# Kernel tuning notes

Measured on AMD Instinct MI355X. Metric: run time of the kernel, lower is better.

## Reference

```python
import jax, jax.numpy as jnp
import numpy as np

NUM_ITERS = 2  # quasi-DEER fixed-point iterations (module default num_iters=2)


def _affine_scan(A, b):
    """Parallel first-order linear recurrence h_t = A_t*h_{t-1} + b_t along axis=1.
    A, b: (B, T, H). Equivalent to torch accelerated-scan after removing pow-2 padding."""
    def comb(l, r):
        A1, b1 = l
        A2, b2 = r
        return A2 * A1, A2 * b1 + b2
    return jax.lax.associative_scan(comb, (A, b), axis=1)[1]


def _run_direction(x, W_in, b_in, W_rec, U_z, b_u, num_iters):
    """quasi-DEER evaluation of a MinRNN layer.
    x: (B, T, d_in). Returns states (B, T, H). Initial state h0 = 0 (hx=None)."""
    B, T, _ = x.shape
    H = b_in.shape[0]
    dtype = x.dtype
    h0 = jnp.zeros((B, H), dtype)
    diag_rec = jnp.diagonal(W_rec)  # (H,)
    # z depends only on the input, not on the state -> precompute once.
    z = jnp.tanh(jnp.einsum('bti,hi->bth', x, W_in) + b_in)  # (B, T, H)
    z0, z_rest = z[:, 0], z[:, 1:]
    states = jnp.zeros((B, T, H), dtype)
    for _ in range(num_iters):
        h_prev = states[:, :-1]  # (B, T-1, H), paired with inputs[:,1:]
        u = jax.nn.sigmoid(jnp.einsum('bth,gh->btg', h_prev, W_rec)
                           + jnp.einsum('bth,gh->btg', z_rest, U_z) + b_u)
        fs = u * h_prev + (1.0 - u) * z_rest                      # cell output f
        As = u + (h_prev - z_rest) * u * (1.0 - u) * diag_rec     # diagonal Jacobian
        bs = fs - As * h_prev
        u0 = jax.nn.sigmoid(h0 @ W_rec.T + z0 @ U_z.T + b_u)
        b0 = u0 * h0 + (1.0 - u0) * z0                            # f(x_0, h0)
        A = jnp.concatenate([jnp.zeros_like(b0)[:, None], As], axis=1)  # A0 = 0
        b = jnp.concatenate([b0[:, None], bs], axis=1)
        states = _affine_scan(A, b)
    return states


def _prnn_forward(input, Wf_in, bf_in, Wf_rec, Uf_z, bf_u,
                  Wb_in, bb_in, Wb_rec, Ub_z, bb_u):
    fwd = _run_direction(input, Wf_in, bf_in, Wf_rec, Uf_z, bf_u, NUM_ITERS)
    bwd = _run_direction(input[:, ::-1], Wb_in, bb_in, Wb_rec, Ub_z, bb_u, NUM_ITERS)[:, ::-1]
    output = jnp.concatenate([fwd, bwd], axis=2)      # (B, T, 2H)
    h_n = jnp.stack([fwd[:, -1], bwd[:, 0]])          # (2, B, H)
    return output, h_n


def setup_inputs() -> dict:
    key = jax.random.key(0)
    ks = jax.random.split(key, 12)
    B, T, D_IN, H = 8, 8192, 256, 256
    def minrnn_params(k0, k1, k2, d_in, h):
        kw, kr, ku = k0, k1, k2
        return dict(
            W_in=jax.random.normal(kw, (h, d_in), jnp.float32) / d_in ** 0.5,
            b_in=jnp.zeros((h,), jnp.float32),
            W_rec=jax.random.normal(kr, (h, h), jnp.float32) / h ** 0.5,
            U_z=jax.random.normal(ku, (h, h), jnp.float32) / h ** 0.5,
            b_u=jnp.zeros((h,), jnp.float32),
        )
    pf = minrnn_params(ks[0], ks[1], ks[2], D_IN, H)
    pb = minrnn_params(ks[3], ks[4], ks[5], D_IN, H)
    return {
        'input': jax.random.normal(ks[6], (B, T, D_IN), jnp.float32),
        'Wf_in': pf['W_in'], 'bf_in': pf['b_in'], 'Wf_rec': pf['W_rec'],
        'Uf_z': pf['U_z'], 'bf_u': pf['b_u'],
        'Wb_in': pb['W_in'], 'bb_in': pb['b_in'], 'Wb_rec': pb['W_rec'],
        'Ub_z': pb['U_z'], 'bb_u': pb['b_u'],
    }


def reference(input, Wf_in, bf_in, Wf_rec, Uf_z, bf_u,
              Wb_in, bb_in, Wb_rec, Ub_z, bb_u):
    return _prnn_forward(input, Wf_in, bf_in, Wf_rec, Uf_z, bf_u,
                         Wb_in, bb_in, Wb_rec, Ub_z, bb_u)
```

## Files before the change

### kernel.cpp

```cpp
#include <hip/hip_runtime.h>
#include <stdint.h>

typedef unsigned short u16;
typedef __attribute__((ext_vector_type(8))) short short8v;
typedef __attribute__((ext_vector_type(4))) short short4v;
typedef __attribute__((ext_vector_type(4))) float f32x4;

#define B_ 8
#define T_ 8192
#define H_ 256
#define M_ 65536
#define MH 16777216
#define NCH 256
#define CHL 32
#define NCHAN 4096

__device__ __forceinline__ u16 f2bf(float f) {
  union { float f; uint32_t u; } v; v.f = f;
  return (u16)((v.u + 0x7FFFu + ((v.u >> 16) & 1u)) >> 16);
}
__device__ __forceinline__ float bf2f(u16 s) {
  union { uint32_t u; float f; } v; v.u = ((uint32_t)s) << 16;
  return v.f;
}
__device__ __forceinline__ float sigm(float x) {
  return __fdividef(1.0f, 1.0f + __expf(-x));
}
__device__ __forceinline__ float tanhfast(float x) {
  return 1.0f - __fdividef(2.0f, __expf(2.0f * x) + 1.0f);
}

__device__ __forceinline__ void compute_Ab(float zf, float ag, float hp, float dr,
                                           float& Aa, float& bb) {
  const float u = sigm(ag);
  const float g = u * (1.f - u) * dr;
  Aa = u + (hp - zf) * g;
  bb = u * hp + (1.f - u) * zf - Aa * hp;
}

__device__ __forceinline__ void g2l16(const void* g, void* l) {
  __builtin_amdgcn_global_load_lds((const __attribute__((address_space(1))) void*)g,
                                   (__attribute__((address_space(3))) void*)l, 16, 0, 0);
}
__device__ __forceinline__ int zts(int row, int col) {
  return row * 256 + ((((col >> 3) ^ (row & 7)) << 3) | (col & 7));
}

__global__ __launch_bounds__(256) void prep_kernel(
    const float* __restrict__ x, u16* __restrict__ xf,
    const float* __restrict__ w0, const float* __restrict__ w1, const float* __restrict__ w2,
    const float* __restrict__ w3, const float* __restrict__ w4, const float* __restrict__ w5,
    u16* __restrict__ wbf) {
  const int bx = blockIdx.x;
  const float* src;
  u16* dst;
  size_t i;
  if (bx < 8192) {
    i = ((size_t)bx * 256 + threadIdx.x) * 8;
    src = x; dst = xf;
  } else {
    const int r = bx - 8192;
    const int wsel = r >> 5, blk = r & 31;
    src = (wsel == 0) ? w0 : (wsel == 1) ? w1 : (wsel == 2) ? w2
        : (wsel == 3) ? w3 : (wsel == 4) ? w4 : w5;
    dst = wbf + (size_t)wsel * 65536;
    i = ((size_t)blk * 256 + threadIdx.x) * 8;
  }
  const float4* s4 = (const float4*)(src + i);
  float4 a = s4[0], b = s4[1];
  short8v o;
  o[0] = (short)f2bf(a.x); o[1] = (short)f2bf(a.y);
  o[2] = (short)f2bf(a.z); o[3] = (short)f2bf(a.w);
  o[4] = (short)f2bf(b.x); o[5] = (short)f2bf(b.y);
  o[6] = (short)f2bf(b.z); o[7] = (short)f2bf(b.w);
  *(short8v*)(dst + i) = o;
}

__global__ __launch_bounds__(256) void zzu_k(
    const u16* __restrict__ xf, const u16* __restrict__ wbf,
    const float* __restrict__ bin0, const float* __restrict__ bin1,
    const float* __restrict__ bu0, const float* __restrict__ bu1,
    const float* __restrict__ Wf_rec, const float* __restrict__ Wb_rec,
    u16* __restrict__ zout, u16* __restrict__ zuout,
    float* __restrict__ Pout, float* __restrict__ qout) {
  __shared__ __align__(16) char lds[65536];
  const int dir = blockIdx.z;
  const int tm = blockIdx.x;
  const char* Win = (const char*)(wbf + (size_t)dir * 196608);
  const char* Uz  = (const char*)(wbf + (size_t)dir * 196608 + 65536);
  const float* bin = dir ? bin1 : bin0;
  const float* bu  = dir ? bu1 : bu0;
  const int tid = threadIdx.x, l = tid & 63, w = tid >> 6;
  const int n0 = w * 64;
  const size_t zoff = (size_t)dir * MH;
  u16* zt  = (u16*)(lds + 32768);
  u16* zut = (u16*)lds;

  f32x4 vzero = {0.f, 0.f, 0.f, 0.f};
  f32x4 acc[4][4];
#pragma unroll
  for (int i = 0; i < 4; ++i)
#pragma unroll
    for (int j = 0; j < 4; ++j) acc[i][j] = vzero;

#pragma unroll
  for (int k0 = 0; k0 < 256; k0 += 64) {
#pragma unroll
    for (int is = 0; is < 2; ++is) {
      const int o = is * 4096 + tid * 16;
      const int row = o >> 7;
      const int cb = (o & 127) ^ ((row & 7) << 4);
      int rA = tm * 64 + row;
      if (dir) { int bb = rA >> 13; int t = rA & 8191; rA = (bb << 13) + (8191 - t); }
      g2l16((const char*)xf + (size_t)rA * 512 + k0 * 2 + cb,
            lds + 32768 + is * 4096 + w * 1024);
    }
#pragma unroll
    for (int is = 0; is < 8; ++is) {
      const int o = is * 4096 + tid * 16;
      const int row = o >> 7;
      const int cb = (o & 127) ^ ((row & 7) << 4);
      g2l16(Win + (size_t)row * 512 + k0 * 2 + cb, lds + is * 4096 + w * 1024);
    }
    __syncthreads();
#pragma unroll
    for (int kk = 0; kk < 2; ++kk) {
      const int colb = (kk * 64 + (l >> 4) * 16) ^ ((l & 7) << 4);
      short8v av[4], bv[4];
#pragma unroll
      for (int i = 0; i < 4; ++i) {
        av[i] = *(const short8v*)(lds + 32768 + (i * 16 + (l & 15)) * 128 + colb);
        bv[i] = *(const short8v*)(lds + (n0 + i * 16 + (l & 15)) * 128 + colb);
      }
#pragma unroll
      for (int i = 0; i < 4; ++i)
#pragma unroll
        for (int j = 0; j < 4; ++j)
          acc[i][j] = __builtin_amdgcn_mfma_f32_16x16x32_bf16(av[i], bv[j], acc[i][j], 0, 0, 0);
    }
    __syncthreads();
  }

#pragma unroll
  for (int j = 0; j < 4; ++j) {
    const int col = n0 + j * 16 + (l & 15);
    const float bv = bin[col];
#pragma unroll
    for (int i = 0; i < 4; ++i)
#pragma unroll
      for (int r = 0; r < 4; ++r) {
        const int row = (l >> 4) * 4 + i * 16 + r;
        zt[zts(row, col)] = f2bf(tanhfast(acc[i][j][r] + bv));
      }
  }
  __syncthreads();

  {
    const int row = tid >> 2;
    const int ub = (tid & 3) * 8;
    char* g = (char*)(zout + zoff) + (size_t)(tm * 64 + row) * 512;
#pragma unroll
    for (int q = 0; q < 8; ++q) {
      const int u = ub + q;
      short8v v = *(const short8v*)((const char*)zt + row * 512 + ((u ^ (row & 7)) << 4));
      *(short8v*)(g + u * 16) = v;
    }
  }

#pragma unroll
  for (int i = 0; i < 4; ++i)
#pragma unroll
    for (int j = 0; j < 4; ++j) acc[i][j] = vzero;
#pragma unroll
  for (int k0 = 0; k0 < 256; k0 += 64) {
#pragma unroll
    for (int is = 0; is < 8; ++is) {
      const int o = is * 4096 + tid * 16;
      const int row = o >> 7;
      const int cb = (o & 127) ^ ((row & 7) << 4);
      g2l16(Uz + (size_t)row * 512 + k0 * 2 + cb, lds + is * 4096 + w * 1024);
    }
    __syncthreads();
#pragma unroll
    for (int kk = 0; kk < 2; ++kk) {
      short8v av[4], bv[4];
#pragma unroll
      for (int i = 0; i < 4; ++i) {
        const int row = i * 16 + (l & 15);
        const int u = (k0 >> 3) + kk * 4 + (l >> 4);
        av[i] = *(const short8v*)((const char*)zt + row * 512 + ((u ^ (row & 7)) << 4));
        const int colb = (kk * 64 + (l >> 4) * 16) ^ ((l & 7) << 4);
        bv[i] = *(const short8v*)(lds + (n0 + i * 16 + (l & 15)) * 128 + colb);
      }
#pragma unroll
      for (int i = 0; i < 4; ++i)
#pragma unroll
        for (int j = 0; j < 4; ++j)
          acc[i][j] = __builtin_amdgcn_mfma_f32_16x16x32_bf16(av[i], bv[j], acc[i][j], 0, 0, 0);
    }
    __syncthreads();
  }

#pragma unroll
  for (int j = 0; j < 4; ++j) {
    const int col = n0 + j * 16 + (l & 15);
    const float bv = bu[col];
#pragma unroll
    for (int i = 0; i < 4; ++i)
#pragma unroll
      for (int r = 0; r < 4; ++r) {
        const int row = (l >> 4) * 4 + i * 16 + r;
        zut[zts(row, col)] = f2bf(acc[i][j][r] + bv);
      }
  }
  __syncthreads();

  {
    const int row = tid >> 2;
    const int ub = (tid & 3) * 8;
    char* g = (char*)(zuout + zoff) + (size_t)(tm * 64 + row) * 512;
#pragma unroll
    for (int q = 0; q < 8; ++q) {
      const int u = ub + q;
      short8v v = *(const short8v*)((const char*)zut + row * 512 + ((u ^ (row & 7)) << 4));
      *(short8v*)(g + u * 16) = v;
    }
  }

  {
    const int h = tid;
    const float dr = (dir ? Wb_rec : Wf_rec)[h * 257];
    const int b = tm >> 7;
    const int c0 = (tm & 127) * 2;
    const int ch = (dir * 8 + b) * 256 + h;
#pragma unroll
    for (int cc = 0; cc < 2; ++cc) {
      float Pv = 1.f, qv = 0.f;
#pragma unroll 4
      for (int it = 0; it < CHL; ++it) {
        const int row = cc * 32 + it;
        const float zf = bf2f(zt[zts(row, h)]);
        const float ag = bf2f(zut[zts(row, h)]);
        float Aa, bbv;
        compute_Ab(zf, ag, 0.f, dr, Aa, bbv);
        qv = Aa * qv + bbv;
        Pv *= Aa;
      }
      Pout[(size_t)(c0 + cc) * NCHAN + ch] = Pv;
      qout[(size_t)(c0 + cc) * NCHAN + ch] = qv;
    }
  }
}

__global__ __launch_bounds__(256) void s1zuh_k(
    const u16* __restrict__ zb, u16* __restrict__ zub,
    const u16* __restrict__ wbf,
    const float* __restrict__ Wf_rec, const float* __restrict__ Wb_rec,
    const float* __restrict__ hst,
    u16* __restrict__ s1out, float* __restrict__ Pout, float* __restrict__ qout) {
  __shared__ __align__(16) char lds[65536];
  const int dir = blockIdx.z;
  const int tm = blockIdx.x;
  const char* Wr = (const char*)(wbf + (size_t)dir * 196608 + 131072);
  const int tid = threadIdx.x, l = tid & 63, w = tid >> 6;
  const int n0 = w * 64;
  const size_t zoff = (size_t)dir * MH;
  u16* s1t = (u16*)(lds + 32768);
  u16* zht = (u16*)lds;

  const int h = tid;
  const float dr = (dir ? Wb_rec : Wf_rec)[h * 257];
  const int b = tm >> 7;
  const int c0 = (tm & 127) * 2;
  const int ch = (dir * 8 + b) * 256 + h;

  s1t[zts(0, h)] = f2bf(hst[(size_t)c0 * NCHAN + ch]);
#pragma unroll
  for (int cc = 0; cc < 2; ++cc) {
    float hcur = hst[(size_t)(c0 + cc) * NCHAN + ch];
#pragma unroll 4
    for (int it = 0; it < CHL; ++it) {
      const size_t g = (size_t)(tm * 64 + cc * 32 + it) * 256 + h;
      const float zf = bf2f(zb[zoff + g]);
      const float ag = bf2f(zub[zoff + g]);
      float Aa, bbv;
      compute_Ab(zf, ag, 0.f, dr, Aa, bbv);
      hcur = Aa * hcur + bbv;
      const int rr = cc * 32 + it + 1;
      if (rr < 64) s1t[zts(rr, h)] = f2bf(hcur);
    }
  }
  __syncthreads();

  {
    const int row = tid >> 2;
    const int ub = (tid & 3) * 8;
    char* g = (char*)(s1out + zoff) + (size_t)(tm * 64 + row) * 512;
#pragma unroll
    for (int q = 0; q < 8; ++q) {
      const int u = ub + q;
      short8v v = *(const short8v*)((const char*)s1t + row * 512 + ((u ^ (row & 7)) << 4));
      *(short8v*)(g + u * 16) = v;
    }
  }

  f32x4 vzero = {0.f, 0.f, 0.f, 0.f};
  f32x4 acc[4][4];
#pragma unroll
  for (int i = 0; i < 4; ++i)
#pragma unroll
    for (int j = 0; j < 4; ++j) acc[i][j] = vzero;
#pragma unroll
  for (int k0 = 0; k0 < 256; k0 += 64) {
#pragma unroll
    for (int is = 0; is < 8; ++is) {
      const int o = is * 4096 + tid * 16;
      const int row = o >> 7;
      const int cb = (o & 127) ^ ((row & 7) << 4);
      g2l16(Wr + (size_t)row * 512 + k0 * 2 + cb, lds + is * 4096 + w * 1024);
    }
    __syncthreads();
#pragma unroll
    for (int kk = 0; kk < 2; ++kk) {
      short8v av[4], bv[4];
#pragma unroll
      for (int i = 0; i < 4; ++i) {
        const int row = i * 16 + (l & 15);
        const int u = (k0 >> 3) + kk * 4 + (l >> 4);
        av[i] = *(const short8v*)((const char*)s1t + row * 512 + ((u ^ (row & 7)) << 4));
        const int colb = (kk * 64 + (l >> 4) * 16) ^ ((l & 7) << 4);
        bv[i] = *(const short8v*)(lds + (n0 + i * 16 + (l & 15)) * 128 + colb);
      }
#pragma unroll
      for (int i = 0; i < 4; ++i)
#pragma unroll
        for (int j = 0; j < 4; ++j)
          acc[i][j] = __builtin_amdgcn_mfma_f32_16x16x32_bf16(av[i], bv[j], acc[i][j], 0, 0, 0);
    }
    __syncthreads();
  }

#pragma unroll
  for (int j = 0; j < 4; ++j) {
    const int col = n0 + j * 16 + (l & 15);
#pragma unroll
    for (int i = 0; i < 4; ++i)
#pragma unroll
      for (int r = 0; r < 4; ++r) {
        const int row = (l >> 4) * 4 + i * 16 + r;
        const float xv = acc[i][j][r] + bf2f(zub[zoff + (size_t)(tm * 64 + row) * 256 + col]);
        zht[zts(row, col)] = f2bf(xv);
      }
  }
  __syncthreads();

  {
    const int row = tid >> 2;
    const int ub = (tid & 3) * 8;
    char* g = (char*)(zub + zoff) + (size_t)(tm * 64 + row) * 512;
#pragma unroll
    for (int q = 0; q < 8; ++q) {
      const int u = ub + q;
      short8v v = *(const short8v*)((const char*)zht + row * 512 + ((u ^ (row & 7)) << 4));
      *(short8v*)(g + u * 16) = v;
    }
  }

#pragma unroll
  for (int cc = 0; cc < 2; ++cc) {
    float Pv = 1.f, qv = 0.f;
#pragma unroll 4
    for (int it = 0; it < CHL; ++it) {
      const int row = cc * 32 + it;
      const float zf = bf2f(zb[zoff + (size_t)(tm * 64 + row) * 256 + h]);
      const float hp = bf2f(s1t[zts(row, h)]);
      const float ag = bf2f(zht[zts(row, h)]);
      float Aa, bbv;
      compute_Ab(zf, ag, hp, dr, Aa, bbv);
      qv = Aa * qv + bbv;
      Pv *= Aa;
    }
    Pout[(size_t)(c0 + cc) * NCHAN + ch] = Pv;
    qout[(size_t)(c0 + cc) * NCHAN + ch] = qv;
  }
}

__global__ __launch_bounds__(256) void scan_p2_kernel(const float* __restrict__ P,
                                                      const float* __restrict__ q,
                                                      float* __restrict__ hstart) {
  const int ch = blockIdx.x * 256 + threadIdx.x;
  float hs = 0.f;
#pragma unroll 8
  for (int c = 0; c < NCH; ++c) {
    hstart[c * NCHAN + ch] = hs;
    hs = P[c * NCHAN + ch] * hs + q[c * NCHAN + ch];
  }
}

__global__ __launch_bounds__(256) void scan_p3_kernel(
    const u16* __restrict__ zb, const u16* __restrict__ zub,
    const u16* __restrict__ s1b,
    const float* __restrict__ Wf_rec, const float* __restrict__ Wb_rec,
    const float* __restrict__ hstart,
    float* __restrict__ out, float* __restrict__ hn) {
  const int wid = blockIdx.x * 4 + (threadIdx.x >> 6);
  const int lane = threadIdx.x & 63;
  const int c = wid & (NCH - 1);
  const int tmp = wid >> 8;
  const int b = tmp & 7;
  const int d = tmp >> 3;
  const int h0 = lane * 4;
  const float* Wr = d ? Wb_rec : Wf_rec;
  float dr[4];
#pragma unroll
  for (int j = 0; j < 4; ++j) dr[j] = Wr[(h0 + j) * 257];
  const size_t off = (size_t)d * MH + ((size_t)b * T_ + (size_t)c * CHL) * H_ + h0;
  const u16* zp = zb + off;
  const u16* zup = zub + off;
  const u16* s1p = s1b + off;
  const int ch0 = (d * 8 + b) * 256 + h0;
  f32x4 h4 = *(const f32x4*)(hstart + (size_t)c * NCHAN + ch0);
  float hc[4] = {h4[0], h4[1], h4[2], h4[3]};
#pragma unroll 4
  for (int it = 0; it < CHL; ++it) {
    const size_t ix = (size_t)it * H_;
    short4v z4 = *(const short4v*)(zp + ix);
    short4v a4 = *(const short4v*)(zup + ix);
    short4v s4 = *(const short4v*)(s1p + ix);
#pragma unroll
    for (int j = 0; j < 4; ++j) {
      const float zf = bf2f((u16)z4[j]);
      const float ag = bf2f((u16)a4[j]);
      const float hp = bf2f((u16)s4[j]);
      float Aa, bb;
      compute_Ab(zf, ag, hp, dr[j], Aa, bb);
      hc[j] = Aa * hc[j] + bb;
    }
    const int t = c * CHL + it;
    const size_t to = (d == 0) ? ((size_t)b * T_ + t) * 512 + h0
                               : ((size_t)b * T_ + (T_ - 1 - t)) * 512 + 256 + h0;
    *(f32x4*)(out + to) = (f32x4){hc[0], hc[1], hc[2], hc[3]};
    if (t == T_ - 1)
      *(f32x4*)(hn + (size_t)(d * 8 + b) * 256 + h0) = (f32x4){hc[0], hc[1], hc[2], hc[3]};
  }
}

extern "C" void kernel_launch(void* const* d_in, const int* in_sizes, int n_in,
                              void* d_out, int out_size, void* d_ws, size_t ws_size,
                              hipStream_t stream) {
  const float* x      = (const float*)d_in[0];
  const float* Wf_in  = (const float*)d_in[1];
  const float* bf_in  = (const float*)d_in[2];
  const float* Wf_rec = (const float*)d_in[3];
  const float* Uf_z   = (const float*)d_in[4];
  const float* bf_u   = (const float*)d_in[5];
  const float* Wb_in  = (const float*)d_in[6];
  const float* bb_in  = (const float*)d_in[7];
  const float* Wb_rec = (const float*)d_in[8];
  const float* Ub_z   = (const float*)d_in[9];
  const float* bb_u   = (const float*)d_in[10];

  char* ws = (char*)d_ws;
  const size_t BF = 33554432;
  u16* xf  = (u16*)(ws + 0 * BF);
  u16* z0  = (u16*)(ws + 1 * BF);
  u16* zu0 = (u16*)(ws + 3 * BF);
  u16* s10 = (u16*)(ws + 5 * BF);
  u16* wbf = (u16*)(ws + 7 * BF);
  char* pb = ws + 7 * BF + 1048576;
  float* Pbuf = (float*)(pb);
  float* qbuf = (float*)(pb + 4194304);
  float* hst  = (float*)(pb + 8388608);
  (void)ws_size; (void)in_sizes; (void)n_in; (void)out_size;

  float* outp = (float*)d_out;
  float* hnp  = outp + (size_t)33554432;

  dim3 gt(1024, 1, 2);

  prep_kernel<<<8384, 256, 0, stream>>>(x, xf, Wf_in, Uf_z, Wf_rec, Wb_in, Ub_z, Wb_rec, wbf);

  zzu_k<<<gt, 256, 0, stream>>>(xf, wbf, bf_in, bb_in, bf_u, bb_u, Wf_rec, Wb_rec,
                                z0, zu0, Pbuf, qbuf);
  scan_p2_kernel<<<16, 256, 0, stream>>>(Pbuf, qbuf, hst);

  s1zuh_k<<<gt, 256, 0, stream>>>(z0, zu0, wbf, Wf_rec, Wb_rec, hst, s10, Pbuf, qbuf);
  scan_p2_kernel<<<16, 256, 0, stream>>>(Pbuf, qbuf, hst);

  scan_p3_kernel<<<1024, 256, 0, stream>>>(z0, zu0, s10, Wf_rec, Wb_rec, hst, outp, hnp);
}
```

Measured before the change: 356.3 us.

## Split fused scan+GEMM into separate scan pass and standalone 128x128 GEMM kernel

The fused s1zuh kernel, which recomputed the first-iteration states per tile and then ran the recurrent GEMM, is replaced by two kernels. A templated scan_p3<1> writes the bf16 first-iteration states, and a new gemm3_k with 128x128 tiles and 512 threads computes the recurrent projection, adds zu, and produces the chunk P/q summaries. The final scan now handles 8 hidden units per lane. This adds a kernel launch and an extra global round trip for s1, in exchange for a larger GEMM tile and a simpler memory layout without swizzling.

```diff
diff --git a/kernel.cpp b/kernel.cpp
--- a/kernel.cpp
+++ b/kernel.cpp
@@ -252,136 +252,115 @@
   }
 }
 
-__global__ __launch_bounds__(256) void s1zuh_k(
-    const u16* __restrict__ zb, u16* __restrict__ zub,
-    const u16* __restrict__ wbf,
-    const float* __restrict__ Wf_rec, const float* __restrict__ Wb_rec,
-    const float* __restrict__ hst,
-    u16* __restrict__ s1out, float* __restrict__ Pout, float* __restrict__ qout) {
-  __shared__ __align__(16) char lds[65536];
-  const int dir = blockIdx.z;
-  const int tm = blockIdx.x;
-  const char* Wr = (const char*)(wbf + (size_t)dir * 196608 + 131072);
-  const int tid = threadIdx.x, l = tid & 63, w = tid >> 6;
-  const int n0 = w * 64;
-  const size_t zoff = (size_t)dir * MH;
-  u16* s1t = (u16*)(lds + 32768);
-  u16* zht = (u16*)lds;
-
-  const int h = tid;
-  const float dr = (dir ? Wb_rec : Wf_rec)[h * 257];
-  const int b = tm >> 7;
-  const int c0 = (tm & 127) * 2;
-  const int ch = (dir * 8 + b) * 256 + h;
-
-  s1t[zts(0, h)] = f2bf(hst[(size_t)c0 * NCHAN + ch]);
-#pragma unroll
-  for (int cc = 0; cc < 2; ++cc) {
-    float hcur = hst[(size_t)(c0 + cc) * NCHAN + ch];
+__global__ __launch_bounds__(512) void gemm3_k(const u16* __restrict__ A,
+                                               const u16* __restrict__ wbf,
+                                               const u16* addm, u16* C,
+                                               const u16* zp_g,
+                                               const float* __restrict__ Wf_rec,
+                                               const float* __restrict__ Wb_rec,
+                                               float* __restrict__ Pout,
+                                               float* __restrict__ qout) {
+  __shared__ __align__(16) char lds[32768];
+  char* ldsA = lds;
+  char* ldsB = lds + 16384;
+  const int bz = blockIdx.z;
+  A += (size_t)bz * (size_t)MH;
+  const u16* Bw = wbf + (size_t)bz * 196608 + 131072;
+  C += (size_t)bz * (size_t)MH;
+  addm += (size_t)bz * (size_t)MH;
+  zp_g += (size_t)bz * (size_t)MH;
+
+  const int tid = threadIdx.x;
+  const int l = tid & 63, w = tid >> 6;
+  const int tm = blockIdx.x, tn = blockIdx.y;
+  const int m0 = (w >> 1) * 32, n0 = (w & 1) * 64;
+  const int wbase = w * 1024;
+
+  f32x4 vzero = {0.f, 0.f, 0.f, 0.f};
+  f32x4 acc[2][4];
+#pragma unroll
+  for (int i = 0; i < 2; ++i)
+#pragma unroll
+    for (int j = 0; j < 4; ++j) acc[i][j] = vzero;
+
+#pragma unroll
+  for (int k0 = 0; k0 < 256; k0 += 64) {
+#pragma unroll
+    for (int is = 0; is < 2; ++is) {
+      const int o = is * 8192 + tid * 16;
+      const int row = o >> 7;
+      const int cb = o & 127;
+      const char* gA = (const char*)A + (size_t)(tm * 128 + row) * 512 + k0 * 2 + cb;
+      g2l16(gA, ldsA + is * 8192 + wbase);
+      const char* gB = (const char*)Bw + (size_t)(tn * 128 + row) * 512 + k0 * 2 + cb;
+      g2l16(gB, ldsB + is * 8192 + wbase);
+    }
+    __syncthreads();
+#pragma unroll
+    for (int ks = 0; ks < 2; ++ks) {
+      short8v av[2], bv[4];
+#pragma unroll
+      for (int i = 0; i < 2; ++i)
+        av[i] = *(const short8v*)(ldsA + (m0 + i * 16 + (l & 15)) * 128 + ks * 64 + (l >> 4) * 16);
+#pragma unroll
+      for (int j = 0; j < 4; ++j)
+        bv[j] = *(const short8v*)(ldsB + (n0 + j * 16 + (l & 15)) * 128 + ks * 64 + (l >> 4) * 16);
+#pragma unroll
+      for (int i = 0; i < 2; ++i)
+#pragma unroll
+        for (int j = 0; j < 4; ++j)
+          acc[i][j] = __builtin_amdgcn_mfma_f32_16x16x32_bf16(av[i], bv[j], acc[i][j], 0, 0, 0);
+    }
+    __syncthreads();
+  }
+
+  u16* lt = (u16*)lds;
+  const int colL = n0 + (l & 15);
+  const int rowL0 = m0 + ((l >> 4) << 2);
+#pragma unroll
+  for (int j = 0; j < 4; ++j) {
+    const int cl = colL + j * 16;
+    const int cg = tn * 128 + cl;
+#pragma unroll
+    for (int i = 0; i < 2; ++i)
+#pragma unroll
+      for (int r = 0; r < 4; ++r) {
+        const int rl = rowL0 + i * 16 + r;
+        float xv = acc[i][j][r] + bf2f(addm[(size_t)(tm * 128 + rl) * 256 + cg]);
+        lt[rl * 128 + cl] = f2bf(xv);
+      }
+  }
+  __syncthreads();
+#pragma unroll
+  for (int itr = 0; itr < 4; ++itr) {
+    const int rl = itr * 32 + (tid >> 4);
+    const int cb = (tid & 15) * 16;
+    short8v v = *(const short8v*)((const char*)lt + rl * 256 + cb);
+    *(short8v*)((char*)C + (size_t)(tm * 128 + rl) * 512 + tn * 256 + cb) = v;
+  }
+
+  {
+    const int cl = tid & 127;
+    const int hg = tn * 128 + cl;
+    const float dr = (bz ? Wb_rec : Wf_rec)[hg * 257];
+    const int bb = (tm * 128) >> 13;
+    const int c0 = ((tm * 128) & 8191) >> 5;
+    const int ch = (bz * 8 + bb) * 256 + hg;
+    const int clc = tid >> 7;
+    float Pv = 1.f, qv = 0.f;
+    const size_t gbase = (size_t)(tm * 128 + clc * CHL) * 256 + hg;
 #pragma unroll 4
     for (int it = 0; it < CHL; ++it) {
-      const size_t g = (size_t)(tm * 64 + cc * 32 + it) * 256 + h;
-      const float zf = bf2f(zb[zoff + g]);
-      const float ag = bf2f(zub[zoff + g]);
-      float Aa, bbv;
-      compute_Ab(zf, ag, 0.f, dr, Aa, bbv);
-      hcur = Aa * hcur + bbv;
-      const int rr = cc * 32 + it + 1;
-      if (rr < 64) s1t[zts(rr, h)] = f2bf(hcur);
-    }
-  }
-  __syncthreads();
-
-  {
-    const int row = tid >> 2;
-    const int ub = (tid & 3) * 8;
-    char* g = (char*)(s1out + zoff) + (size_t)(tm * 64 + row) * 512;
-#pragma unroll
-    for (int q = 0; q < 8; ++q) {
-      const int u = ub + q;
-      short8v v = *(const short8v*)((const char*)s1t + row * 512 + ((u ^ (row & 7)) << 4));
-      *(short8v*)(g + u * 16) = v;
-    }
-  }
-
-  f32x4 vzero = {0.f, 0.f, 0.f, 0.f};
-  f32x4 acc[4][4];
-#pragma unroll
-  for (int i = 0; i < 4; ++i)
-#pragma unroll
-    for (int j = 0; j < 4; ++j) acc[i][j] = vzero;
-#pragma unroll
-  for (int k0 = 0; k0 < 256; k0 += 64) {
-#pragma unroll
-    for (int is = 0; is < 8; ++is) {
-      const int o = is * 4096 + tid * 16;
-      const int row = o >> 7;
-      const int cb = (o & 127) ^ ((row & 7) << 4);
-      g2l16(Wr + (size_t)row * 512 + k0 * 2 + cb, lds + is * 4096 + w * 1024);
-    }
-    __syncthreads();
-#pragma unroll
-    for (int kk = 0; kk < 2; ++kk) {
-      short8v av[4], bv[4];
-#pragma unroll
-      for (int i = 0; i < 4; ++i) {
-        const int row = i * 16 + (l & 15);
-        const int u = (k0 >> 3) + kk * 4 + (l >> 4);
-        av[i] = *(const short8v*)((const char*)s1t + row * 512 + ((u ^ (row & 7)) << 4));
-        const int colb = (kk * 64 + (l >> 4) * 16) ^ ((l & 7) << 4);
-        bv[i] = *(const short8v*)(lds + (n0 + i * 16 + (l & 15)) * 128 + colb);
-      }
-#pragma unroll
-      for (int i = 0; i < 4; ++i)
-#pragma unroll
-        for (int j = 0; j < 4; ++j)
-          acc[i][j] = __builtin_amdgcn_mfma_f32_16x16x32_bf16(av[i], bv[j], acc[i][j], 0, 0, 0);
-    }
-    __syncthreads();
-  }
-
-#pragma unroll
-  for (int j = 0; j < 4; ++j) {
-    const int col = n0 + j * 16 + (l & 15);
-#pragma unroll
-    for (int i = 0; i < 4; ++i)
-#pragma unroll
-      for (int r = 0; r < 4; ++r) {
-        const int row = (l >> 4) * 4 + i * 16 + r;
-        const float xv = acc[i][j][r] + bf2f(zub[zoff + (size_t)(tm * 64 + row) * 256 + col]);
-        zht[zts(row, col)] = f2bf(xv);
-      }
-  }
-  __syncthreads();
-
-  {
-    const int row = tid >> 2;
-    const int ub = (tid & 3) * 8;
-    char* g = (char*)(zub + zoff) + (size_t)(tm * 64 + row) * 512;
-#pragma unroll
-    for (int q = 0; q < 8; ++q) {
-      const int u = ub + q;
-      short8v v = *(const short8v*)((const char*)zht + row * 512 + ((u ^ (row & 7)) << 4));
-      *(short8v*)(g + u * 16) = v;
-    }
-  }
-
-#pragma unroll
-  for (int cc = 0; cc < 2; ++cc) {
-    float Pv = 1.f, qv = 0.f;
-#pragma unroll 4
-    for (int it = 0; it < CHL; ++it) {
-      const int row = cc * 32 + it;
-      const float zf = bf2f(zb[zoff + (size_t)(tm * 64 + row) * 256 + h]);
-      const float hp = bf2f(s1t[zts(row, h)]);
-      const float ag = bf2f(zht[zts(row, h)]);
+      const float ag = bf2f(lt[(clc * CHL + it) * 128 + cl]);
+      const float zf = bf2f(zp_g[gbase + (size_t)it * 256]);
+      const float hp = bf2f(A[gbase + (size_t)it * 256]);
       float Aa, bbv;
       compute_Ab(zf, ag, hp, dr, Aa, bbv);
       qv = Aa * qv + bbv;
       Pv *= Aa;
     }
-    Pout[(size_t)(c0 + cc) * NCHAN + ch] = Pv;
-    qout[(size_t)(c0 + cc) * NCHAN + ch] = qv;
+    Pout[(size_t)(c0 + clc) * NCHAN + ch] = Pv;
+    qout[(size_t)(c0 + clc) * NCHAN + ch] = qv;
   }
 }
 
@@ -397,51 +376,74 @@
   }
 }
 
+template <int ITER>
 __global__ __launch_bounds__(256) void scan_p3_kernel(
     const u16* __restrict__ zb, const u16* __restrict__ zub,
     const u16* __restrict__ s1b,
     const float* __restrict__ Wf_rec, const float* __restrict__ Wb_rec,
     const float* __restrict__ hstart,
-    float* __restrict__ out, float* __restrict__ hn) {
-  const int wid = blockIdx.x * 4 + (threadIdx.x >> 6);
+    u16* __restrict__ s1out, float* __restrict__ out, float* __restrict__ hn) {
+  const int unit = blockIdx.x * 4 + (threadIdx.x >> 6);
   const int lane = threadIdx.x & 63;
-  const int c = wid & (NCH - 1);
-  const int tmp = wid >> 8;
-  const int b = tmp & 7;
-  const int d = tmp >> 3;
-  const int h0 = lane * 4;
+  const int cpair = unit & 127;
+  const int seq = unit >> 7;
+  const int b = seq & 7;
+  const int d = seq >> 3;
+  const int c = cpair * 2 + (lane >> 5);
+  const int h0 = (lane & 31) * 8;
   const float* Wr = d ? Wb_rec : Wf_rec;
-  float dr[4];
-#pragma unroll
-  for (int j = 0; j < 4; ++j) dr[j] = Wr[(h0 + j) * 257];
+  float dr[8];
+#pragma unroll
+  for (int j = 0; j < 8; ++j) dr[j] = Wr[(h0 + j) * 257];
   const size_t off = (size_t)d * MH + ((size_t)b * T_ + (size_t)c * CHL) * H_ + h0;
   const u16* zp = zb + off;
   const u16* zup = zub + off;
   const u16* s1p = s1b + off;
   const int ch0 = (d * 8 + b) * 256 + h0;
-  f32x4 h4 = *(const f32x4*)(hstart + (size_t)c * NCHAN + ch0);
-  float hc[4] = {h4[0], h4[1], h4[2], h4[3]};
-#pragma unroll 4
+  float hc[8];
+  {
+    f32x4 ha = *(const f32x4*)(hstart + (size_t)c * NCHAN + ch0);
+    f32x4 hb = *(const f32x4*)(hstart + (size_t)c * NCHAN + ch0 + 4);
+#pragma unroll
+    for (int j = 0; j < 4; ++j) { hc[j] = ha[j]; hc[4 + j] = hb[j]; }
+  }
+  if (ITER == 1 && c == 0) {
+    *(short8v*)(s1out + off) = (short8v){0, 0, 0, 0, 0, 0, 0, 0};
+  }
+#pragma unroll 8
   for (int it = 0; it < CHL; ++it) {
     const size_t ix = (size_t)it * H_;
-    short4v z4 = *(const short4v*)(zp + ix);
-    short4v a4 = *(const short4v*)(zup + ix);
-    short4v s4 = *(const short4v*)(s1p + ix);
-#pragma unroll
-    for (int j = 0; j < 4; ++j) {
-      const float zf = bf2f((u16)z4[j]);
-      const float ag = bf2f((u16)a4[j]);
-      const float hp = bf2f((u16)s4[j]);
+    short8v z8 = *(const short8v*)(zp + ix);
+    short8v a8 = *(const short8v*)(zup + ix);
+    short8v s8 = {0, 0, 0, 0, 0, 0, 0, 0};
+    if (ITER == 2) s8 = *(const short8v*)(s1p + ix);
+#pragma unroll
+    for (int j = 0; j < 8; ++j) {
+      const float zf = bf2f((u16)z8[j]);
+      const float ag = bf2f((u16)a8[j]);
+      const float hp = (ITER == 2) ? bf2f((u16)s8[j]) : 0.f;
       float Aa, bb;
       compute_Ab(zf, ag, hp, dr[j], Aa, bb);
       hc[j] = Aa * hc[j] + bb;
     }
     const int t = c * CHL + it;
-    const size_t to = (d == 0) ? ((size_t)b * T_ + t) * 512 + h0
-                               : ((size_t)b * T_ + (T_ - 1 - t)) * 512 + 256 + h0;
-    *(f32x4*)(out + to) = (f32x4){hc[0], hc[1], hc[2], hc[3]};
-    if (t == T_ - 1)
-      *(f32x4*)(hn + (size_t)(d * 8 + b) * 256 + h0) = (f32x4){hc[0], hc[1], hc[2], hc[3]};
+    if (ITER == 1) {
+      if (t < T_ - 1) {
+        short8v o;
+#pragma unroll
+        for (int j = 0; j < 8; ++j) o[j] = (short)f2bf(hc[j]);
+        *(short8v*)(s1out + off + ix + H_) = o;
+      }
+    } else {
+      const size_t to = (d == 0) ? ((size_t)b * T_ + t) * 512 + h0
+                                 : ((size_t)b * T_ + (T_ - 1 - t)) * 512 + 256 + h0;
+      *(f32x4*)(out + to)     = (f32x4){hc[0], hc[1], hc[2], hc[3]};
+      *(f32x4*)(out + to + 4) = (f32x4){hc[4], hc[5], hc[6], hc[7]};
+      if (t == T_ - 1) {
+        *(f32x4*)(hn + (size_t)(d * 8 + b) * 256 + h0)     = (f32x4){hc[0], hc[1], hc[2], hc[3]};
+        *(f32x4*)(hn + (size_t)(d * 8 + b) * 256 + h0 + 4) = (f32x4){hc[4], hc[5], hc[6], hc[7]};
+      }
+    }
   }
 }
 
@@ -476,16 +478,20 @@
   float* outp = (float*)d_out;
   float* hnp  = outp + (size_t)33554432;
 
+  prep_kernel<<<8384, 256, 0, stream>>>(x, xf, Wf_in, Uf_z, Wf_rec, Wb_in, Ub_z, Wb_rec, wbf);
+
   dim3 gt(1024, 1, 2);
-
-  prep_kernel<<<8384, 256, 0, stream>>>(x, xf, Wf_in, Uf_z, Wf_rec, Wb_in, Ub_z, Wb_rec, wbf);
-
   zzu_k<<<gt, 256, 0, stream>>>(xf, wbf, bf_in, bb_in, bf_u, bb_u, Wf_rec, Wb_rec,
                                 z0, zu0, Pbuf, qbuf);
+
   scan_p2_kernel<<<16, 256, 0, stream>>>(Pbuf, qbuf, hst);
-
-  s1zuh_k<<<gt, 256, 0, stream>>>(z0, zu0, wbf, Wf_rec, Wb_rec, hst, s10, Pbuf, qbuf);
+  scan_p3_kernel<1><<<512, 256, 0, stream>>>(z0, zu0, s10, Wf_rec, Wb_rec, hst,
+                                             s10, nullptr, nullptr);
+
+  dim3 gg(512, 2, 2);
+  gemm3_k<<<gg, 512, 0, stream>>>(s10, wbf, zu0, zu0, z0, Wf_rec, Wb_rec, Pbuf, qbuf);
+
   scan_p2_kernel<<<16, 256, 0, stream>>>(Pbuf, qbuf, hst);
-
-  scan_p3_kernel<<<1024, 256, 0, stream>>>(z0, zu0, s10, Wf_rec, Wb_rec, hst, outp, hnp);
-}
+  scan_p3_kernel<2><<<512, 256, 0, stream>>>(z0, zu0, s10, Wf_rec, Wb_rec, hst,
+                                             nullptr, outp, hnp);
+}
```

Result: faster. 341.3 us (-4.2%).
